# Performance work log

Hardware: AMD Instinct MI355X
Metric: run time of the kernel (lower is better)

The kernel has to match this reference:

```python
import jax, jax.numpy as jnp
import numpy as np

B, E, S = 32768, 256, 1024  # batch, embedding dim, n speakers (32 utterances/speaker)
EPS_COS = 1e-8    # torch cosine_similarity eps
EPS_NORM = 1e-12  # F.normalize eps


def setup_inputs() -> dict:
    key = jax.random.key(0)
    k1, = jax.random.split(key, 1)
    inputs = jax.random.normal(k1, (B, E), dtype=jnp.float32)
    # balanced speakers so every speaker id in [0,S) is present
    targets = jnp.repeat(jnp.arange(S, dtype=jnp.int32), B // S)
    w = jnp.asarray(1.0, dtype=jnp.float32)  # nn.Parameter init 1.0
    b = jnp.asarray(0.0, dtype=jnp.float32)  # nn.Parameter init 0.0
    return {"inputs": inputs, "targets": targets, "w": w, "b": b}


def _ge2e(inputs, targets, w, b):
    # Faithful to source: per-speaker .sum() collapses BOTH utterance and
    # embedding dims to a SCALAR (a quirk/bug of the original, reproduced here).
    row_sum = inputs.sum(axis=1)                                   # [B]
    s = jax.ops.segment_sum(row_sum, targets, num_segments=S)     # [S] scalar sum per speaker
    n = jax.ops.segment_sum(jnp.ones_like(row_sum), targets, num_segments=S)  # [S] counts

    w_relu = jax.nn.relu(w)
    norm_e = jnp.linalg.norm(inputs, axis=1)                       # [B]

    # leave-one-out 'centroid': (scalar_sum - e) / n_j, broadcast to [B,E]
    s_j = s[targets]
    n_j = n[targets]
    cms = (s_j[:, None] - inputs) / n_j[:, None]                   # [B,E]
    norm_c = jnp.linalg.norm(cms, axis=1)                          # [B]
    self_cos = jnp.sum(inputs * cms, axis=1) / (
        jnp.maximum(norm_e, EPS_COS) * jnp.maximum(norm_c, EPS_COS))
    self_sim = w_relu * self_cos + b                               # [B]

    # other-speaker 'centroid' is a scalar c_k = s_k / n_k, broadcast to ones(E)*c_k
    c = s / n                                                      # [S]
    norm_ck = jnp.abs(c) * jnp.sqrt(jnp.asarray(E, inputs.dtype))  # [S]
    cos_other = (row_sum[:, None] * c[None, :]) / (
        jnp.maximum(norm_e, EPS_COS)[:, None] * jnp.maximum(norm_ck, EPS_COS)[None, :])
    sim = w_relu * cos_other + b                                   # [B,S]
    # own-speaker slot uses the leave-one-out similarity
    sim = sim.at[jnp.arange(B), targets].set(self_sim)

    loss = jnp.sum(-self_sim + jax.scipy.special.logsumexp(sim, axis=1))
    normalized = inputs / jnp.maximum(norm_e, EPS_NORM)[:, None]
    return normalized, loss


def reference(inputs, targets, w, b):
    normalized, loss = _ge2e(inputs, targets, w, b)
    return (normalized, loss)
```

## Files before the change

### kernel.cpp

```cpp
#include <hip/hip_runtime.h>
#include <math.h>

#define B_ 32768
#define E_ 256
#define S_ 1024
#define EPS_COS 1e-8f
#define EPS_NORM 1e-12f

typedef float fx4 __attribute__((ext_vector_type(4)));

__global__ __launch_bounds__(256) void rows_kernel(
        const float* __restrict__ x, const int* __restrict__ tgt,
        float* __restrict__ outN, float* __restrict__ outL,
        float* __restrict__ rowsum, float* __restrict__ sqsum,
        float* __restrict__ PBsum, int* __restrict__ PBtgt) {
    __shared__ float sSum[16];
    __shared__ int   sTgt[16];

    int tid = threadIdx.x;
    int g   = tid >> 4;
    int li  = tid & 15;
    int row = blockIdx.x * 16 + g;

    if (blockIdx.x == 0 && tid == 0) outL[0] = 0.f;

    const fx4* __restrict__ xr = (const fx4*)(x + (size_t)row * E_);
    fx4* __restrict__ orow = (fx4*)(outN + (size_t)row * E_);

    fx4 a0 = xr[li];
    fx4 a1 = xr[li + 16];
    fx4 a2 = xr[li + 32];
    fx4 a3 = xr[li + 48];

    float sum = (a0.x + a0.y + a0.z + a0.w) + (a1.x + a1.y + a1.z + a1.w)
              + (a2.x + a2.y + a2.z + a2.w) + (a3.x + a3.y + a3.z + a3.w);
    float sq  = (a0.x*a0.x + a0.y*a0.y + a0.z*a0.z + a0.w*a0.w)
              + (a1.x*a1.x + a1.y*a1.y + a1.z*a1.z + a1.w*a1.w)
              + (a2.x*a2.x + a2.y*a2.y + a2.z*a2.z + a2.w*a2.w)
              + (a3.x*a3.x + a3.y*a3.y + a3.z*a3.z + a3.w*a3.w);

    #pragma unroll
    for (int o = 8; o >= 1; o >>= 1) {
        sum += __shfl_xor(sum, o, 64);
        sq  += __shfl_xor(sq,  o, 64);
    }

    float rn = 1.0f / fmaxf(sqrtf(sq), EPS_NORM);
    __builtin_nontemporal_store(a0 * rn, &orow[li]);
    __builtin_nontemporal_store(a1 * rn, &orow[li + 16]);
    __builtin_nontemporal_store(a2 * rn, &orow[li + 32]);
    __builtin_nontemporal_store(a3 * rn, &orow[li + 48]);

    if (li == 0) {
        rowsum[row] = sum;
        sqsum[row]  = sq;
        sSum[g] = sum;
        sTgt[g] = tgt[row];
    }
    __syncthreads();
    if (tid == 0) {
        float tot = 0.f;
        int t0 = sTgt[0];
        int same = 1;
        #pragma unroll
        for (int k = 0; k < 16; ++k) {
            tot += sSum[k];
            same &= (sTgt[k] == t0);
        }
        PBsum[blockIdx.x] = tot;
        PBtgt[blockIdx.x] = same ? t0 : -1;
    }
}

__global__ __launch_bounds__(256) void loss_kernel(
        const float* __restrict__ rowsum, const float* __restrict__ sqsum,
        const int* __restrict__ tgt,
        const float* __restrict__ PBsum, const int* __restrict__ PBtgt,
        const float* __restrict__ wP, const float* __restrict__ bP,
        float* __restrict__ outL) {
    __shared__ float s_h[S_];
    __shared__ float c_h[S_];
    __shared__ int   ired[256];
    __shared__ float fred[256];

    int tid = threadIdx.x;

    int packed = 0;
    int bad = 0;
    #pragma unroll
    for (int j = 0; j < 4; ++j) {
        int k = tid * 4 + j;
        float sk = PBsum[2*k] + PBsum[2*k+1];
        int ok = (PBtgt[2*k] == k) & (PBtgt[2*k+1] == k);
        bad |= !ok;
        s_h[k] = sk;
        c_h[k] = 32.0f;
        float cv = sk * (1.0f / 32.0f);
        if (fabsf(cv) * 16.0f >= EPS_COS) packed += (cv > 0.f) ? (1 << 16) : 1;
    }
    ired[tid] = packed | (bad ? (1 << 15) : 0);
    __syncthreads();
    #pragma unroll
    for (int st = 128; st > 0; st >>= 1) {
        if (tid < st) {
            int a = ired[tid], b = ired[tid + st];
            ired[tid] = ((a + b) & ~(1 << 15)) | ((a | b) & (1 << 15));
        }
        __syncthreads();
    }
    int agg  = ired[0];
    int slow = (agg >> 15) & 1;
    int npos = (agg >> 16) & 0xFFFF;
    int nneg = agg & 0x7FFF;

    if (slow) {
        __syncthreads();
        s_h[tid] = 0.f; s_h[tid + 256] = 0.f; s_h[tid + 512] = 0.f; s_h[tid + 768] = 0.f;
        c_h[tid] = 0.f; c_h[tid + 256] = 0.f; c_h[tid + 512] = 0.f; c_h[tid + 768] = 0.f;
        __syncthreads();
        for (int i = tid; i < B_; i += 256) {
            int t = tgt[i];
            atomicAdd(&s_h[t], rowsum[i]);
            atomicAdd(&c_h[t], 1.0f);
        }
        __syncthreads();
        packed = 0;
        #pragma unroll
        for (int j = 0; j < 4; ++j) {
            int k = tid * 4 + j;
            float cv = s_h[k] / c_h[k];
            if (fabsf(cv) * 16.0f >= EPS_COS) packed += (cv > 0.f) ? (1 << 16) : 1;
        }
        ired[tid] = packed;
        __syncthreads();
        #pragma unroll
        for (int st = 128; st > 0; st >>= 1) {
            if (tid < st) ired[tid] += ired[tid + st];
            __syncthreads();
        }
        npos = ired[0] >> 16;
        nneg = ired[0] & 0xFFFF;
    }

    int i = blockIdx.x * 256 + tid;
    float w  = wP[0], b = bP[0];
    float wr = fmaxf(w, 0.f);

    int   t  = tgt[i];
    float rs = rowsum[i], sq = sqsum[i];
    float sj = s_h[t], nj = c_h[t];

    float nem = fmaxf(sqrtf(sq), EPS_COS);

    float dot = (sj * rs - sq) / nj;
    float nc  = sqrtf((float)E_ * sj * sj - 2.f * sj * rs + sq) / nj;
    float self_cos = dot / (nem * fmaxf(nc, EPS_COS));
    float self_sim = wr * self_cos + b;

    float A  = wr * rs / (nem * 16.0f);
    float xp =  A + b, xm = -A + b, xz = b;

    float ct = sj / nj;
    int np = npos, nm = nneg, nz = S_ - npos - nneg;
    if (fabsf(ct) * 16.0f >= EPS_COS) { if (ct > 0.f) np--; else nm--; }
    else nz--;

    float m = self_sim;
    if (np > 0) m = fmaxf(m, xp);
    if (nm > 0) m = fmaxf(m, xm);
    if (nz > 0) m = fmaxf(m, xz);
    float ssum = expf(self_sim - m)
               + (float)np * expf(xp - m)
               + (float)nm * expf(xm - m)
               + (float)nz * expf(xz - m);
    float contrib = m + logf(ssum) - self_sim;

    fred[tid] = contrib;
    __syncthreads();
    #pragma unroll
    for (int st = 128; st > 0; st >>= 1) {
        if (tid < st) fred[tid] += fred[tid + st];
        __syncthreads();
    }
    if (tid == 0) atomicAdd(outL, fred[0]);
}

extern "C" void kernel_launch(void* const* d_in, const int* in_sizes, int n_in,
                              void* d_out, int out_size, void* d_ws, size_t ws_size,
                              hipStream_t stream) {
    const float* inputs  = (const float*)d_in[0];
    const int*   targets = (const int*)d_in[1];
    const float* wP      = (const float*)d_in[2];
    const float* bP      = (const float*)d_in[3];
    float* outN = (float*)d_out;
    float* outL = (float*)d_out + (size_t)B_ * E_;

    float* wsf    = (float*)d_ws;
    float* rowsum = wsf;
    float* sqsum  = wsf + B_;
    float* PBsum  = wsf + 2 * B_;
    int*   PBtgt  = (int*)(PBsum + 2048);

    rows_kernel<<<B_ / 16, 256, 0, stream>>>(inputs, targets, outN, outL,
                                             rowsum, sqsum, PBsum, PBtgt);
    loss_kernel<<<B_ / 256, 256, 0, stream>>>(rowsum, sqsum, targets,
                                              PBsum, PBtgt, wP, bP, outL);
}
```

Baseline: 19.75 us.

## Split row reduction and normalization into separate kernels

Splits the fused row kernel into two. The first reads the inputs and writes only row sums, squared norms and per-block partial sums. A new scale kernel then re-reads the inputs, loads the precomputed norms and writes the normalized output with nontemporal stores. This adds a second full pass over the 32 MB input and an extra launch, possibly in exchange for a lighter reduction kernel and better-coalesced stores, but the extra traffic is likely to dominate.

```diff
diff --git a/kernel.cpp b/kernel.cpp
--- a/kernel.cpp
+++ b/kernel.cpp
@@ -9,9 +9,9 @@
 
 typedef float fx4 __attribute__((ext_vector_type(4)));
 
-__global__ __launch_bounds__(256) void rows_kernel(
+__global__ __launch_bounds__(256) void reduce_kernel(
         const float* __restrict__ x, const int* __restrict__ tgt,
-        float* __restrict__ outN, float* __restrict__ outL,
+        float* __restrict__ outL,
         float* __restrict__ rowsum, float* __restrict__ sqsum,
         float* __restrict__ PBsum, int* __restrict__ PBtgt) {
     __shared__ float sSum[16];
@@ -25,7 +25,6 @@
     if (blockIdx.x == 0 && tid == 0) outL[0] = 0.f;
 
     const fx4* __restrict__ xr = (const fx4*)(x + (size_t)row * E_);
-    fx4* __restrict__ orow = (fx4*)(outN + (size_t)row * E_);
 
     fx4 a0 = xr[li];
     fx4 a1 = xr[li + 16];
@@ -44,12 +43,6 @@
         sum += __shfl_xor(sum, o, 64);
         sq  += __shfl_xor(sq,  o, 64);
     }
-
-    float rn = 1.0f / fmaxf(sqrtf(sq), EPS_NORM);
-    __builtin_nontemporal_store(a0 * rn, &orow[li]);
-    __builtin_nontemporal_store(a1 * rn, &orow[li + 16]);
-    __builtin_nontemporal_store(a2 * rn, &orow[li + 32]);
-    __builtin_nontemporal_store(a3 * rn, &orow[li + 48]);
 
     if (li == 0) {
         rowsum[row] = sum;
@@ -70,6 +63,33 @@
         PBsum[blockIdx.x] = tot;
         PBtgt[blockIdx.x] = same ? t0 : -1;
     }
+}
+
+__global__ __launch_bounds__(256) void scale_kernel(
+        const float* __restrict__ x, const float* __restrict__ sqsum,
+        float* __restrict__ outN) {
+    int tid  = threadIdx.x;
+    int w    = tid >> 6;
+    int l    = tid & 63;
+    int row0 = blockIdx.x * 16 + w * 4;
+
+    const fx4* __restrict__ x0 = (const fx4*)(x + (size_t)row0 * E_);
+    fx4* __restrict__ o0 = (fx4*)(outN + (size_t)row0 * E_);
+
+    fx4 a0 = x0[l];
+    fx4 a1 = x0[l + 64];
+    fx4 a2 = x0[l + 128];
+    fx4 a3 = x0[l + 192];
+
+    float r0 = 1.0f / fmaxf(sqrtf(sqsum[row0]),     EPS_NORM);
+    float r1 = 1.0f / fmaxf(sqrtf(sqsum[row0 + 1]), EPS_NORM);
+    float r2 = 1.0f / fmaxf(sqrtf(sqsum[row0 + 2]), EPS_NORM);
+    float r3 = 1.0f / fmaxf(sqrtf(sqsum[row0 + 3]), EPS_NORM);
+
+    __builtin_nontemporal_store(a0 * r0, &o0[l]);
+    __builtin_nontemporal_store(a1 * r1, &o0[l + 64]);
+    __builtin_nontemporal_store(a2 * r2, &o0[l + 128]);
+    __builtin_nontemporal_store(a3 * r3, &o0[l + 192]);
 }
 
 __global__ __launch_bounds__(256) void loss_kernel(
@@ -201,8 +221,9 @@
     float* PBsum  = wsf + 2 * B_;
     int*   PBtgt  = (int*)(PBsum + 2048);
 
-    rows_kernel<<<B_ / 16, 256, 0, stream>>>(inputs, targets, outN, outL,
-                                             rowsum, sqsum, PBsum, PBtgt);
+    reduce_kernel<<<B_ / 16, 256, 0, stream>>>(inputs, targets, outL,
+                                               rowsum, sqsum, PBsum, PBtgt);
+    scale_kernel<<<B_ / 16, 256, 0, stream>>>(inputs, sqsum, outN);
     loss_kernel<<<B_ / 256, 256, 0, stream>>>(rowsum, sqsum, targets,
                                               PBsum, PBtgt, wP, bP, outL);
 }
```

Result: slower. 23.51 us (+19.1%).
